# Optimization experiments

Hardware: AMD Instinct MI355X
Metric: run time of the kernel (lower is better)

## Reference

```python
import jax, jax.numpy as jnp
import numpy as np

N_NODES = 50000
N_EDGES = 800000
IN_DIM = 3
OUT_DIM = 50


def _glorot(key, shape):
    fan_in, fan_out = shape[0], shape[1]
    lim = np.sqrt(6.0 / (fan_in + fan_out))
    return jax.random.uniform(key, shape, jnp.float32, -lim, lim)


def setup_inputs() -> dict:
    key = jax.random.key(0)
    ks = jax.random.split(key, 16)
    x = jax.random.normal(ks[0], (N_NODES, IN_DIM), jnp.float32)
    edge_index = jax.random.randint(ks[1], (2, N_EDGES), 0, N_NODES, jnp.int64)
    return {
        "x": x,
        "edge_index": edge_index,
        # pointwise Conv1d (kernel_size=1) == per-node Linear; store as [in, out]
        "w1": _glorot(ks[2], (IN_DIM, 32)), "b1": jnp.zeros((32,), jnp.float32),
        "w2": _glorot(ks[3], (32, 64)),     "b2": jnp.zeros((64,), jnp.float32),
        "w3": _glorot(ks[4], (64, 128)),    "b3": jnp.zeros((128,), jnp.float32),
        # GCNConv weights [in, out] + bias
        "g1w": _glorot(ks[5], (128, 256)),  "g1b": jnp.zeros((256,), jnp.float32),
        "g2w": _glorot(ks[6], (256, 512)),  "g2b": jnp.zeros((512,), jnp.float32),
        "g3w": _glorot(ks[7], (512, OUT_DIM)), "g3b": jnp.zeros((OUT_DIM,), jnp.float32),
    }


def _gcn_conv(h, src, dst, dinv, W, b):
    """PyG GCNConv: add self-loops + symmetric norm. h: [N, Fin]."""
    n = h.shape[0]
    h = h @ W  # [N, Fout]
    norm = dinv[src] * dinv[dst]  # [E]
    msg = h[src] * norm[:, None]  # gather over edges [E, Fout]
    agg = jax.ops.segment_sum(msg, dst, num_segments=n)
    # self-loop contribution: norm = dinv[i]^2
    agg = agg + h * (dinv * dinv)[:, None]
    return agg + b


def reference(x, edge_index, w1, b1, w2, b2, w3, b3, g1w, g1b, g2w, g2b, g3w, g3b):
    src, dst = edge_index[0], edge_index[1]
    n = x.shape[0]
    # degree with self-loops (in-degree on targets), shared by all GCN layers
    deg = jnp.zeros((n,), x.dtype).at[dst].add(1.0) + 1.0
    dinv = jax.lax.rsqrt(deg)

    # pointwise conv stack (1x1 Conv1d == per-node dense layer)
    h = jax.nn.relu(x @ w1 + b1)
    h = jax.nn.relu(h @ w2 + b2)
    h = jax.nn.relu(h @ w3 + b3)

    h = jax.nn.relu(_gcn_conv(h, src, dst, dinv, g1w, g1b))
    h = jax.nn.relu(_gcn_conv(h, src, dst, dinv, g2w, g2b))
    h = _gcn_conv(h, src, dst, dinv, g3w, g3b)
    return jax.nn.softmax(h, axis=1)  # [N, OUT_DIM]
```

## Files before the change

### kernel.cpp

```cpp
#include <hip/hip_runtime.h>
#include <hip/hip_bf16.h>
#include <math.h>


typedef __attribute__((ext_vector_type(8))) short short8;
typedef __attribute__((ext_vector_type(8))) _Float16 half8;
typedef __attribute__((ext_vector_type(4))) float floatx4;

__device__ __forceinline__ unsigned short bf16h(float f) {
    unsigned int u = __float_as_uint(f);
    u += 0x7fff + ((u >> 16) & 1);
    return (unsigned short)(u >> 16);
}
__device__ __forceinline__ float bf16f(unsigned short h) {
    return __uint_as_float(((unsigned int)h) << 16);
}

__device__ __forceinline__ void gld_lds16(unsigned short* lds, const unsigned short* g) {
    __builtin_amdgcn_global_load_lds(
        (const __attribute__((address_space(1))) unsigned int*)g,
        (__attribute__((address_space(3))) unsigned int*)lds, 16, 0, 0);
}


__global__ void hist_kernel(const int* __restrict__ dst, int* __restrict__ counts, int e) {
    int g = blockIdx.x * blockDim.x + threadIdx.x;
    if (g < e) atomicAdd(&counts[dst[g]], 1);
}

__global__ void scan1_kernel(const int* __restrict__ counts, int* __restrict__ bsum, int n) {
    __shared__ int buf[256];
    int i = blockIdx.x * 256 + threadIdx.x;
    buf[threadIdx.x] = (i < n) ? counts[i] : 0;
    __syncthreads();
    for (int off = 128; off > 0; off >>= 1) {
        if (threadIdx.x < off) buf[threadIdx.x] += buf[threadIdx.x + off];
        __syncthreads();
    }
    if (threadIdx.x == 0) bsum[blockIdx.x] = buf[0];
}

__global__ void scan2_kernel(const int* __restrict__ bsum, int* __restrict__ bsumx,
                             int* __restrict__ offsets, int nb, int n) {
    __shared__ int buf[256];
    int tid = threadIdx.x;
    int v = (tid < nb) ? bsum[tid] : 0;
    buf[tid] = v;
    __syncthreads();
    for (int off = 1; off < 256; off <<= 1) {
        int t = (tid >= off) ? buf[tid - off] : 0;
        __syncthreads();
        buf[tid] += t;
        __syncthreads();
    }
    if (tid < nb) bsumx[tid] = buf[tid] - v;
    if (tid == 255) offsets[n] = buf[255];
}

__global__ void scan3_kernel(const int* __restrict__ counts, const int* __restrict__ bsumx,
                             int* __restrict__ offsets, int* __restrict__ cursor,
                             float* __restrict__ dinv, int n) {
    __shared__ int buf[256];
    int tid = threadIdx.x;
    int i = blockIdx.x * 256 + tid;
    int c = (i < n) ? counts[i] : 0;
    buf[tid] = c;
    __syncthreads();
    for (int off = 1; off < 256; off <<= 1) {
        int t = (tid >= off) ? buf[tid - off] : 0;
        __syncthreads();
        buf[tid] += t;
        __syncthreads();
    }
    if (i < n) {
        int excl = bsumx[blockIdx.x] + buf[tid] - c;
        offsets[i] = excl;
        cursor[i] = excl;
        dinv[i] = rsqrtf((float)c + 1.0f);
    }
}

__global__ void fill_kernel(const int* __restrict__ src, const int* __restrict__ dst,
                            const float* __restrict__ dinv, int* __restrict__ cursor,
                            int* __restrict__ ssrc, float* __restrict__ snorm, int e) {
    int g = blockIdx.x * blockDim.x + threadIdx.x;
    if (g >= e) return;
    int s = src[g], d = dst[g];
    int pos = atomicAdd(&cursor[d], 1);
    ssrc[pos]  = s;
    snorm[pos] = dinv[s] * dinv[d];
}


__global__ void prepw_kernel(const float* __restrict__ g1w, const float* __restrict__ g2w,
                             const float* __restrict__ g3w, const float* __restrict__ w3,
                             _Float16* __restrict__ Bt1f,
                             _Float16* __restrict__ Bt2f,
                             unsigned short* __restrict__ Bt3,
                             _Float16* __restrict__ Bt0f) {
    int gid = blockIdx.x * blockDim.x + threadIdx.x;
    if (gid < 32768) {
        int k = gid >> 8, n = gid & 255;
        Bt1f[(size_t)n * 128 + k] = (_Float16)g1w[gid];
    } else if (gid < 32768 + 131072) {
        int idx = gid - 32768;
        int k = idx >> 9, n = idx & 511;
        Bt2f[(size_t)n * 256 + k] = (_Float16)g2w[idx];
    } else if (gid < 32768 + 131072 + 32768) {
        int idx = gid - 32768 - 131072;
        int k = idx >> 6, c = idx & 63;
        float w = (c < 50) ? g3w[k * 50 + c] : 0.0f;
        unsigned short h = bf16h(w);
        unsigned short l = bf16h(w - bf16f(h));
        size_t base = (size_t)c * 1024;
        Bt3[base + k]       = h;
        Bt3[base + 512 + k] = l;
    } else if (gid < 32768 + 131072 + 32768 + 8192) {
        int idx = gid - 32768 - 131072 - 32768;
        int k = idx >> 7, n = idx & 127;
        Bt0f[(size_t)n * 64 + k] = (_Float16)w3[idx];
    }
}


__global__ __launch_bounds__(256) void mlp12_kernel(
        const float* __restrict__ x,
        const float* __restrict__ w1, const float* __restrict__ b1,
        const float* __restrict__ w2, const float* __restrict__ b2,
        _Float16* __restrict__ H2f, int n) {
    __shared__ float sw1[96], sb1[32], sw2[2048], sb2[64];
    int tid = threadIdx.x;
    if (tid < 96) sw1[tid] = w1[tid];
    if (tid < 32) sb1[tid] = b1[tid];
    if (tid < 64) sb2[tid] = b2[tid];
    for (int i = tid; i < 2048; i += 256) sw2[i] = w2[i];
    __syncthreads();

    int node = blockIdx.x * 256 + tid;
    if (node >= n) return;
    float x0 = x[node * 3 + 0], x1 = x[node * 3 + 1], x2 = x[node * 3 + 2];
    float h1[32];
#pragma unroll
    for (int j = 0; j < 32; j++)
        h1[j] = fmaxf(sb1[j] + x0 * sw1[j] + x1 * sw1[32 + j] + x2 * sw1[64 + j], 0.0f);

    float acc[64];
#pragma unroll
    for (int j = 0; j < 64; j++) acc[j] = sb2[j];
    for (int k = 0; k < 32; k++) {
        float hk = h1[k];
#pragma unroll
        for (int j4 = 0; j4 < 16; j4++) {
            float4 w = *(const float4*)&sw2[k * 64 + j4 * 4];
            acc[j4 * 4 + 0] = fmaf(hk, w.x, acc[j4 * 4 + 0]);
            acc[j4 * 4 + 1] = fmaf(hk, w.y, acc[j4 * 4 + 1]);
            acc[j4 * 4 + 2] = fmaf(hk, w.z, acc[j4 * 4 + 2]);
            acc[j4 * 4 + 3] = fmaf(hk, w.w, acc[j4 * 4 + 3]);
        }
    }
#pragma unroll
    for (int j8 = 0; j8 < 8; j8++) {
        half8 o;
#pragma unroll
        for (int t = 0; t < 8; t++)
            o[t] = (_Float16)fmaxf(acc[j8 * 8 + t], 0.0f);
        *reinterpret_cast<half8*>(&H2f[(size_t)node * 64 + j8 * 8]) = o;
    }
}


template<int BM, int BN, int WAVES, int WGR, int WGC, int WRF, int WCF, int SWIZCOLS>
__global__ __launch_bounds__(WAVES * 64) void gemm_f16_kernel(
        const _Float16* __restrict__ A, const _Float16* __restrict__ Btf,
        const float* __restrict__ bias, _Float16* __restrict__ C,
        int M, int K, int N) {
    static_assert(WGR * WRF * 16 == BM, "row cover");
    static_assert(WGC * WCF * 16 == BN, "col cover");
    static_assert(WGR * WGC == WAVES, "wave grid");
    constexpr int AUNITS = BM / 16, BUNITS = BN / 16;
    static_assert(AUNITS % WAVES == 0 && BUNITS % WAVES == 0, "staging split");
    __shared__ __align__(16) unsigned short Ash[BM * 32];
    __shared__ __align__(16) unsigned short Bsh[BN * 32];

    int bm, bn;
    if (SWIZCOLS > 0) {
        constexpr int CSH = (SWIZCOLS == 4) ? 2 : 1;
        int b = blockIdx.x;
        int col = (b >> 3) & (SWIZCOLS - 1);
        int row = ((b >> (3 + CSH)) << 3) | (b & 7);
        bm = row * BM;
        bn = col * BN;
        if (bm >= M) return;
    } else {
        bm = blockIdx.y * BM;
        bn = blockIdx.x * BN;
    }

    const int tid  = threadIdx.x;
    const int lane = tid & 63;
    const int wave = tid >> 6;
    const int wr0 = (wave / WGC) * (WRF * 16);
    const int wc0 = (wave % WGC) * (WCF * 16);
    const int lr   = lane & 15;
    const int quad = lane >> 4;
    const int arow = lane >> 2;
    const int acol = (lane & 3) * 8;

    floatx4 acc[WRF][WCF];
#pragma unroll
    for (int i = 0; i < WRF; i++)
#pragma unroll
        for (int j = 0; j < WCF; j++) acc[i][j] = floatx4{0.f, 0.f, 0.f, 0.f};

    for (int k0 = 0; k0 < K; k0 += 32) {
#pragma unroll
        for (int u = 0; u < AUNITS / WAVES; u++) {
            int grp = wave + u * WAVES;
            int gm = bm + grp * 16 + arow;
            if (gm >= M) gm = M - 1;
            gld_lds16(&Ash[grp * 512],
                      (const unsigned short*)(A + (size_t)gm * K + k0 + acol));
        }
#pragma unroll
        for (int u = 0; u < BUNITS / WAVES; u++) {
            int grp = wave + u * WAVES;
            int gr = bn + grp * 16 + arow;
            gld_lds16(&Bsh[grp * 512],
                      (const unsigned short*)(Btf + (size_t)gr * K + k0 + acol));
        }
        __syncthreads();

        half8 af[WRF], bf[WCF];
#pragma unroll
        for (int i = 0; i < WRF; i++)
            af[i] = *reinterpret_cast<const half8*>(
                &Ash[(wr0 + i * 16 + lr) * 32 + quad * 8]);
#pragma unroll
        for (int j = 0; j < WCF; j++)
            bf[j] = *reinterpret_cast<const half8*>(
                &Bsh[(wc0 + j * 16 + lr) * 32 + quad * 8]);
#pragma unroll
        for (int i = 0; i < WRF; i++)
#pragma unroll
            for (int j = 0; j < WCF; j++)
                acc[i][j] = __builtin_amdgcn_mfma_f32_16x16x32_f16(
                    af[i], bf[j], acc[i][j], 0, 0, 0);
        __syncthreads();
    }

#pragma unroll
    for (int i = 0; i < WRF; i++) {
#pragma unroll
        for (int j = 0; j < WCF; j++) {
            int gc = bn + wc0 + j * 16 + lr;
#pragma unroll
            for (int reg = 0; reg < 4; reg++) {
                int gr = bm + wr0 + i * 16 + quad * 4 + reg;
                if (gr >= M) continue;
                float v = fmaxf(acc[i][j][reg] + bias[gc], 0.0f);
                C[(size_t)gr * N + gc] = (_Float16)v;
            }
        }
    }
}


template<int BM, int BN, int WAVES, int WGR, int WGC, int WRF, int WCF>
__global__ __launch_bounds__(WAVES * 64) void gemm_emul_kernel(
        const _Float16* __restrict__ Af, const unsigned short* __restrict__ Bt,
        _Float16* __restrict__ C, int M, int K, int N) {
    static_assert(WGR * WRF * 16 == BM, "row cover");
    static_assert(WGC * WCF * 16 == BN, "col cover");
    static_assert(WGR * WGC == WAVES, "wave grid");
    constexpr int AUNITS = BM / 16, BUNITS = BN / 8;
    static_assert(AUNITS % WAVES == 0 && BUNITS % WAVES == 0, "staging split");
    __shared__ __align__(16) unsigned short Ash[BM * 32];
    __shared__ __align__(16) unsigned short Bsh[BN * 32];
    __shared__ __align__(16) unsigned short Bsl[BN * 32];

    const int bm = blockIdx.y * BM;
    const int bn = blockIdx.x * BN;
    const int tid  = threadIdx.x;
    const int lane = tid & 63;
    const int wave = tid >> 6;
    const int K2 = 2 * K;
    const int wr0 = (wave / WGC) * (WRF * 16);
    const int wc0 = (wave % WGC) * (WCF * 16);
    const int lr   = lane & 15;
    const int quad = lane >> 4;
    const int arow = lane >> 2;
    const int acol = (lane & 3) * 8;

    floatx4 acc[WRF][WCF];
#pragma unroll
    for (int i = 0; i < WRF; i++)
#pragma unroll
        for (int j = 0; j < WCF; j++) acc[i][j] = floatx4{0.f, 0.f, 0.f, 0.f};

    for (int k0 = 0; k0 < K; k0 += 32) {
#pragma unroll
        for (int u = 0; u < AUNITS / WAVES; u++) {
            int grp = wave + u * WAVES;
            int gm = bm + grp * 16 + arow;
            if (gm >= M) gm = M - 1;
            gld_lds16(&Ash[grp * 512],
                      (const unsigned short*)(Af + (size_t)gm * K + k0 + acol));
        }
#pragma unroll
        for (int u = 0; u < BUNITS / WAVES; u++) {
            int unit = wave + u * WAVES;
            int grp = unit >> 1, pl = unit & 1;
            int gr = bn + grp * 16 + arow;
            size_t go = (size_t)gr * K2 + k0 + acol + (pl ? K : 0);
            if (pl) gld_lds16(&Bsl[grp * 512], Bt + go);
            else    gld_lds16(&Bsh[grp * 512], Bt + go);
        }
        __syncthreads();

        short8 ahf[WRF], alf[WRF], bhf[WCF], blf[WCF];
#pragma unroll
        for (int i = 0; i < WRF; i++) {
            half8 av = *reinterpret_cast<const half8*>(
                &Ash[(wr0 + i * 16 + lr) * 32 + quad * 8]);
#pragma unroll
            for (int t = 0; t < 8; t++) {
                float f = (float)av[t];
                unsigned short h = bf16h(f);
                ahf[i][t] = (short)h;
                alf[i][t] = (short)bf16h(f - bf16f(h));
            }
        }
#pragma unroll
        for (int j = 0; j < WCF; j++) {
            int ro = (wc0 + j * 16 + lr) * 32 + quad * 8;
            bhf[j] = *reinterpret_cast<const short8*>(&Bsh[ro]);
            blf[j] = *reinterpret_cast<const short8*>(&Bsl[ro]);
        }
#pragma unroll
        for (int i = 0; i < WRF; i++)
#pragma unroll
            for (int j = 0; j < WCF; j++) {
                acc[i][j] = __builtin_amdgcn_mfma_f32_16x16x32_bf16(
                    ahf[i], bhf[j], acc[i][j], 0, 0, 0);
                acc[i][j] = __builtin_amdgcn_mfma_f32_16x16x32_bf16(
                    ahf[i], blf[j], acc[i][j], 0, 0, 0);
                acc[i][j] = __builtin_amdgcn_mfma_f32_16x16x32_bf16(
                    alf[i], bhf[j], acc[i][j], 0, 0, 0);
            }
        __syncthreads();
    }

#pragma unroll
    for (int i = 0; i < WRF; i++) {
#pragma unroll
        for (int j = 0; j < WCF; j++) {
            int gc = bn + wc0 + j * 16 + lr;
#pragma unroll
            for (int reg = 0; reg < 4; reg++) {
                int gr = bm + wr0 + i * 16 + quad * 4 + reg;
                if (gr >= M) continue;
                C[(size_t)gr * N + gc] = (_Float16)acc[i][j][reg];
            }
        }
    }
}


template<int F>
__global__ void agg_f16_kernel(const _Float16* __restrict__ table,
                               const int* __restrict__ offsets,
                               const int* __restrict__ ssrc,
                               const float* __restrict__ snorm,
                               const float* __restrict__ dinv,
                               _Float16* __restrict__ Aout, int n) {
    constexpr int F8 = F / 8;
    int gid = blockIdx.x * blockDim.x + threadIdx.x;
    if (gid >= n * F8) return;
    int node = gid / F8;
    int c8 = (gid - node * F8) * 8;

    float acc[8];
#pragma unroll
    for (int i = 0; i < 8; i++) acc[i] = 0.0f;

    int beg = offsets[node], end = offsets[node + 1];
    for (int e = beg; e < end; ++e) {
        int s = ssrc[e];
        float w = snorm[e];
        half8 r = *reinterpret_cast<const half8*>(table + (size_t)s * F + c8);
#pragma unroll
        for (int i = 0; i < 8; i++) acc[i] = fmaf((float)r[i], w, acc[i]);
    }
    float dv = dinv[node];
    float sw = dv * dv;
    half8 r = *reinterpret_cast<const half8*>(table + (size_t)node * F + c8);
#pragma unroll
    for (int i = 0; i < 8; i++) acc[i] = fmaf((float)r[i], sw, acc[i]);

    half8 o;
#pragma unroll
    for (int i = 0; i < 8; i++) o[i] = (_Float16)acc[i];
    *reinterpret_cast<half8*>(&Aout[(size_t)node * F + c8]) = o;
}


__global__ void agg50_softmax_kernel(const _Float16* __restrict__ z,
                                     const int* __restrict__ offsets,
                                     const int* __restrict__ ssrc,
                                     const float* __restrict__ snorm,
                                     const float* __restrict__ dinv,
                                     const float* __restrict__ bias,
                                     float* __restrict__ out, int n) {
    int node = blockIdx.x * 4 + (threadIdx.x >> 6);
    int lane = threadIdx.x & 63;
    if (node >= n) return;

    float a0 = 0.f, a1 = 0.f, a2 = 0.f, a3 = 0.f;
    int beg = offsets[node], end = offsets[node + 1];
    int e = beg;
    for (; e + 4 <= end; e += 4) {
        int s0 = ssrc[e + 0], s1 = ssrc[e + 1], s2 = ssrc[e + 2], s3 = ssrc[e + 3];
        float w0 = snorm[e + 0], w1 = snorm[e + 1];
        float w2 = snorm[e + 2], w3 = snorm[e + 3];
        float r0 = (float)z[(size_t)s0 * 64 + lane];
        float r1 = (float)z[(size_t)s1 * 64 + lane];
        float r2 = (float)z[(size_t)s2 * 64 + lane];
        float r3 = (float)z[(size_t)s3 * 64 + lane];
        a0 = fmaf(r0, w0, a0);
        a1 = fmaf(r1, w1, a1);
        a2 = fmaf(r2, w2, a2);
        a3 = fmaf(r3, w3, a3);
    }
    for (; e < end; ++e)
        a0 = fmaf((float)z[(size_t)ssrc[e] * 64 + lane], snorm[e], a0);

    float dv = dinv[node];
    float a = fmaf((float)z[(size_t)node * 64 + lane], dv * dv,
                   (a0 + a1) + (a2 + a3));

    float v = (lane < 50) ? a + bias[lane] : -INFINITY;
    float m = v;
#pragma unroll
    for (int off = 32; off > 0; off >>= 1) m = fmaxf(m, __shfl_xor(m, off));
    float ex = (lane < 50) ? expf(v - m) : 0.0f;
    float s = ex;
#pragma unroll
    for (int off = 32; off > 0; off >>= 1) s += __shfl_xor(s, off);
    if (lane < 50) out[(size_t)node * 50 + lane] = ex / s;
}


extern "C" void kernel_launch(void* const* d_in, const int* in_sizes, int n_in,
                              void* d_out, int out_size, void* d_ws, size_t ws_size,
                              hipStream_t stream) {
    const float* x    = (const float*)d_in[0];
    const int*   ei   = (const int*)  d_in[1];
    const float* w1   = (const float*)d_in[2];
    const float* b1   = (const float*)d_in[3];
    const float* w2   = (const float*)d_in[4];
    const float* b2   = (const float*)d_in[5];
    const float* w3   = (const float*)d_in[6];
    const float* b3   = (const float*)d_in[7];
    const float* g1w  = (const float*)d_in[8];
    const float* g1b  = (const float*)d_in[9];
    const float* g2w  = (const float*)d_in[10];
    const float* g2b  = (const float*)d_in[11];
    const float* g3w  = (const float*)d_in[12];
    const float* g3b  = (const float*)d_in[13];
    float* out = (float*)d_out;

    const int N = in_sizes[0] / 3;
    const int E = in_sizes[1] / 2;
    const int* src = ei;
    const int* dst = ei + E;
    const int NB = (N + 255) / 256;

    char* ws = (char*)d_ws;
    size_t off = 0;
    auto alloc = [&](size_t bytes) -> char* {
        char* p = ws + off;
        off = (off + bytes + 255) & ~(size_t)255;
        return p;
    };
    int*   counts  = (int*)  alloc((size_t)N * 4);
    int*   offsets = (int*)  alloc((size_t)(N + 1) * 4);
    int*   cursor  = (int*)  alloc((size_t)N * 4);
    float* dinv    = (float*)alloc((size_t)N * 4);
    int*   bsum    = (int*)  alloc((size_t)256 * 4);
    int*   bsumx   = (int*)  alloc((size_t)256 * 4);
    int*   ssrc    = (int*)  alloc((size_t)E * 4);
    float* snorm   = (float*)alloc((size_t)E * 4);
    _Float16* Bt1f = (_Float16*)alloc((size_t)256 * 128 * 2);
    _Float16* Bt2f = (_Float16*)alloc((size_t)512 * 256 * 2);
    unsigned short* Bt3 = (unsigned short*)alloc((size_t)64 * 1024 * 2);
    _Float16* Bt0f = (_Float16*)alloc((size_t)128 * 64 * 2);
    char* R1 = alloc((size_t)N * 256 * 4);
    char* R2 = alloc((size_t)N * 256 * 4);
    char* R3 = alloc((size_t)N * 512 * 2);
    (void)ws_size;

    _Float16*       S128f = (_Float16*)R1;
    _Float16*       A128f = (_Float16*)(R1 + (size_t)N * 128 * 2);
    _Float16*       A256f = (_Float16*)R1;
    _Float16*       H2f  = (_Float16*)R2;
    _Float16*       G1f  = (_Float16*)R2;
    _Float16*       zbuf = (_Float16*)R2;
    _Float16*       A512f = (_Float16*)R3;

    hipMemsetAsync(counts, 0, (size_t)N * 4, stream);
    hist_kernel<<<(E + 255) / 256, 256, 0, stream>>>(dst, counts, E);
    scan1_kernel<<<NB, 256, 0, stream>>>(counts, bsum, N);
    scan2_kernel<<<1, 256, 0, stream>>>(bsum, bsumx, offsets, NB, N);
    scan3_kernel<<<NB, 256, 0, stream>>>(counts, bsumx, offsets, cursor, dinv, N);
    fill_kernel<<<(E + 255) / 256, 256, 0, stream>>>(src, dst, dinv, cursor, ssrc, snorm, E);
    prepw_kernel<<<(204800 + 255) / 256, 256, 0, stream>>>(
        g1w, g2w, g3w, w3, Bt1f, Bt2f, Bt3, Bt0f);

    const int MB = (N + 127) / 128;
    const int MB8 = (MB + 7) & ~7;
    const int MB64 = (N + 63) / 64;

    mlp12_kernel<<<NB, 256, 0, stream>>>(x, w1, b1, w2, b2, H2f, N);
    {   dim3 grid(1, MB);
        gemm_f16_kernel<128, 128, 4, 2, 2, 4, 4, 0><<<grid, 256, 0, stream>>>(
            H2f, Bt0f, b3, S128f, N, 64, 128);
    }

    agg_f16_kernel<128><<<((size_t)N * 16 + 255) / 256, 256, 0, stream>>>(
        S128f, offsets, ssrc, snorm, dinv, A128f, N);
    gemm_f16_kernel<128, 128, 4, 2, 2, 4, 4, 2><<<2 * MB8, 256, 0, stream>>>(
        A128f, Bt1f, g1b, G1f, N, 128, 256);

    agg_f16_kernel<256><<<((size_t)N * 32 + 255) / 256, 256, 0, stream>>>(
        G1f, offsets, ssrc, snorm, dinv, A256f, N);
    gemm_f16_kernel<128, 128, 4, 2, 2, 4, 4, 4><<<4 * MB8, 256, 0, stream>>>(
        A256f, Bt2f, g2b, A512f, N, 256, 512);

    {   dim3 grid(1, MB64);
        gemm_emul_kernel<64, 64, 4, 4, 1, 1, 4><<<grid, 256, 0, stream>>>(
            A512f, Bt3, zbuf, N, 512, 64);
    }
    agg50_softmax_kernel<<<(N + 3) / 4, 256, 0, stream>>>(
        zbuf, offsets, ssrc, snorm, dinv, g3b, out, N);
}
```

Baseline: 453.9 us.

## Partition aggregation by feature slice per XCC with work-stealing queues and packed edges

After: 921.7 us. +103.1%, slower.

```diff
diff --git a/kernel.cpp b/kernel.cpp
--- a/kernel.cpp
+++ b/kernel.cpp
@@ -6,6 +6,8 @@
 typedef __attribute__((ext_vector_type(8))) short short8;
 typedef __attribute__((ext_vector_type(8))) _Float16 half8;
 typedef __attribute__((ext_vector_type(4))) float floatx4;
+
+#define XCC_ID_IMM 6164
 
 __device__ __forceinline__ unsigned short bf16h(float f) {
     unsigned int u = __float_as_uint(f);
@@ -82,13 +84,12 @@
 
 __global__ void fill_kernel(const int* __restrict__ src, const int* __restrict__ dst,
                             const float* __restrict__ dinv, int* __restrict__ cursor,
-                            int* __restrict__ ssrc, float* __restrict__ snorm, int e) {
+                            int2* __restrict__ edges, int e) {
     int g = blockIdx.x * blockDim.x + threadIdx.x;
     if (g >= e) return;
     int s = src[g], d = dst[g];
     int pos = atomicAdd(&cursor[d], 1);
-    ssrc[pos]  = s;
-    snorm[pos] = dinv[s] * dinv[d];
+    edges[pos] = make_int2(s, __float_as_int(dinv[s] * dinv[d]));
 }
 
 
@@ -367,47 +368,90 @@
 
 
 template<int F>
-__global__ void agg_f16_kernel(const _Float16* __restrict__ table,
-                               const int* __restrict__ offsets,
-                               const int* __restrict__ ssrc,
-                               const float* __restrict__ snorm,
-                               const float* __restrict__ dinv,
-                               _Float16* __restrict__ Aout, int n) {
-    constexpr int F8 = F / 8;
-    int gid = blockIdx.x * blockDim.x + threadIdx.x;
-    if (gid >= n * F8) return;
-    int node = gid / F8;
-    int c8 = (gid - node * F8) * 8;
-
-    float acc[8];
-#pragma unroll
-    for (int i = 0; i < 8; i++) acc[i] = 0.0f;
-
-    int beg = offsets[node], end = offsets[node + 1];
-    for (int e = beg; e < end; ++e) {
-        int s = ssrc[e];
-        float w = snorm[e];
-        half8 r = *reinterpret_cast<const half8*>(table + (size_t)s * F + c8);
-#pragma unroll
-        for (int i = 0; i < 8; i++) acc[i] = fmaf((float)r[i], w, acc[i]);
-    }
-    float dv = dinv[node];
-    float sw = dv * dv;
-    half8 r = *reinterpret_cast<const half8*>(table + (size_t)node * F + c8);
-#pragma unroll
-    for (int i = 0; i < 8; i++) acc[i] = fmaf((float)r[i], sw, acc[i]);
-
-    half8 o;
-#pragma unroll
-    for (int i = 0; i < 8; i++) o[i] = (_Float16)acc[i];
-    *reinterpret_cast<half8*>(&Aout[(size_t)node * F + c8]) = o;
+__global__ __launch_bounds__(256) void agg_slice_kernel(
+        const _Float16* __restrict__ table,
+        const int* __restrict__ offsets,
+        const int2* __restrict__ edges,
+        const float* __restrict__ dinv,
+        _Float16* __restrict__ Aout,
+        int* __restrict__ qheads, int n) {
+    constexpr int SF  = F / 8;
+    constexpr int LPN = SF / 8;
+    constexpr int NPB = 256 / LPN;
+    const int nslabs = (n + NPB - 1) / NPB;
+
+    __shared__ int sx, sslab;
+    const int tid = threadIdx.x;
+    if (tid == 0) sx = __builtin_amdgcn_s_getreg(XCC_ID_IMM) & 7;
+    __syncthreads();
+    const int myx = sx;
+    const int sub = tid & (LPN - 1);
+    const int nid = tid / LPN;
+
+    for (int t = 0; t < 8; t++) {
+        int q = (myx + t) & 7;
+        const int f0 = q * SF + sub * 8;
+        while (true) {
+            if (tid == 0) sslab = atomicAdd(&qheads[q], 1);
+            __syncthreads();
+            int slab = sslab;
+            __syncthreads();
+            if (slab >= nslabs) break;
+            int node = slab * NPB + nid;
+            if (node < n) {
+                float a0[8], a1[8];
+#pragma unroll
+                for (int i = 0; i < 8; i++) { a0[i] = 0.f; a1[i] = 0.f; }
+                int beg = offsets[node], end = offsets[node + 1];
+                int e = beg;
+                for (; e + 4 <= end; e += 4) {
+                    int2 E0 = edges[e + 0], E1 = edges[e + 1];
+                    int2 E2 = edges[e + 2], E3 = edges[e + 3];
+                    half8 r0 = *reinterpret_cast<const half8*>(
+                        table + (size_t)E0.x * F + f0);
+                    half8 r1 = *reinterpret_cast<const half8*>(
+                        table + (size_t)E1.x * F + f0);
+                    half8 r2 = *reinterpret_cast<const half8*>(
+                        table + (size_t)E2.x * F + f0);
+                    half8 r3 = *reinterpret_cast<const half8*>(
+                        table + (size_t)E3.x * F + f0);
+                    float w0 = __int_as_float(E0.y), w1 = __int_as_float(E1.y);
+                    float w2 = __int_as_float(E2.y), w3 = __int_as_float(E3.y);
+#pragma unroll
+                    for (int i = 0; i < 8; i++) {
+                        a0[i] = fmaf((float)r0[i], w0, a0[i]);
+                        a1[i] = fmaf((float)r1[i], w1, a1[i]);
+                        a0[i] = fmaf((float)r2[i], w2, a0[i]);
+                        a1[i] = fmaf((float)r3[i], w3, a1[i]);
+                    }
+                }
+                for (; e < end; ++e) {
+                    int2 E0 = edges[e];
+                    half8 r0 = *reinterpret_cast<const half8*>(
+                        table + (size_t)E0.x * F + f0);
+                    float w0 = __int_as_float(E0.y);
+#pragma unroll
+                    for (int i = 0; i < 8; i++)
+                        a0[i] = fmaf((float)r0[i], w0, a0[i]);
+                }
+                float dv = dinv[node];
+                float sw = dv * dv;
+                half8 rs = *reinterpret_cast<const half8*>(
+                    table + (size_t)node * F + f0);
+                half8 o;
+#pragma unroll
+                for (int i = 0; i < 8; i++)
+                    o[i] = (_Float16)fmaf((float)rs[i], sw, a0[i] + a1[i]);
+                *reinterpret_cast<half8*>(&Aout[(size_t)node * F + f0]) = o;
+            }
+        }
+    }
 }
 
 
 __global__ void agg50_softmax_kernel(const _Float16* __restrict__ z,
                                      const int* __restrict__ offsets,
-                                     const int* __restrict__ ssrc,
-                                     const float* __restrict__ snorm,
+                                     const int2* __restrict__ edges,
                                      const float* __restrict__ dinv,
                                      const float* __restrict__ bias,
                                      float* __restrict__ out, int n) {
@@ -419,20 +463,21 @@
     int beg = offsets[node], end = offsets[node + 1];
     int e = beg;
     for (; e + 4 <= end; e += 4) {
-        int s0 = ssrc[e + 0], s1 = ssrc[e + 1], s2 = ssrc[e + 2], s3 = ssrc[e + 3];
-        float w0 = snorm[e + 0], w1 = snorm[e + 1];
-        float w2 = snorm[e + 2], w3 = snorm[e + 3];
-        float r0 = (float)z[(size_t)s0 * 64 + lane];
-        float r1 = (float)z[(size_t)s1 * 64 + lane];
-        float r2 = (float)z[(size_t)s2 * 64 + lane];
-        float r3 = (float)z[(size_t)s3 * 64 + lane];
-        a0 = fmaf(r0, w0, a0);
-        a1 = fmaf(r1, w1, a1);
-        a2 = fmaf(r2, w2, a2);
-        a3 = fmaf(r3, w3, a3);
-    }
-    for (; e < end; ++e)
-        a0 = fmaf((float)z[(size_t)ssrc[e] * 64 + lane], snorm[e], a0);
+        int2 E0 = edges[e + 0], E1 = edges[e + 1];
+        int2 E2 = edges[e + 2], E3 = edges[e + 3];
+        float r0 = (float)z[(size_t)E0.x * 64 + lane];
+        float r1 = (float)z[(size_t)E1.x * 64 + lane];
+        float r2 = (float)z[(size_t)E2.x * 64 + lane];
+        float r3 = (float)z[(size_t)E3.x * 64 + lane];
+        a0 = fmaf(r0, __int_as_float(E0.y), a0);
+        a1 = fmaf(r1, __int_as_float(E1.y), a1);
+        a2 = fmaf(r2, __int_as_float(E2.y), a2);
+        a3 = fmaf(r3, __int_as_float(E3.y), a3);
+    }
+    for (; e < end; ++e) {
+        int2 E0 = edges[e];
+        a0 = fmaf((float)z[(size_t)E0.x * 64 + lane], __int_as_float(E0.y), a0);
+    }
 
     float dv = dinv[node];
     float a = fmaf((float)z[(size_t)node * 64 + lane], dv * dv,
@@ -483,13 +528,13 @@
         return p;
     };
     int*   counts  = (int*)  alloc((size_t)N * 4);
+    int*   qheads  = (int*)  alloc((size_t)16 * 4);
     int*   offsets = (int*)  alloc((size_t)(N + 1) * 4);
     int*   cursor  = (int*)  alloc((size_t)N * 4);
     float* dinv    = (float*)alloc((size_t)N * 4);
     int*   bsum    = (int*)  alloc((size_t)256 * 4);
     int*   bsumx   = (int*)  alloc((size_t)256 * 4);
-    int*   ssrc    = (int*)  alloc((size_t)E * 4);
-    float* snorm   = (float*)alloc((size_t)E * 4);
+    int2*  edges   = (int2*) alloc((size_t)E * 8);
     _Float16* Bt1f = (_Float16*)alloc((size_t)256 * 128 * 2);
     _Float16* Bt2f = (_Float16*)alloc((size_t)512 * 256 * 2);
     unsigned short* Bt3 = (unsigned short*)alloc((size_t)64 * 1024 * 2);
@@ -508,11 +553,12 @@
     _Float16*       A512f = (_Float16*)R3;
 
     hipMemsetAsync(counts, 0, (size_t)N * 4, stream);
+    hipMemsetAsync(qheads, 0, 64, stream);
     hist_kernel<<<(E + 255) / 256, 256, 0, stream>>>(dst, counts, E);
     scan1_kernel<<<NB, 256, 0, stream>>>(counts, bsum, N);
     scan2_kernel<<<1, 256, 0, stream>>>(bsum, bsumx, offsets, NB, N);
     scan3_kernel<<<NB, 256, 0, stream>>>(counts, bsumx, offsets, cursor, dinv, N);
-    fill_kernel<<<(E + 255) / 256, 256, 0, stream>>>(src, dst, dinv, cursor, ssrc, snorm, E);
+    fill_kernel<<<(E + 255) / 256, 256, 0, stream>>>(src, dst, dinv, cursor, edges, E);
     prepw_kernel<<<(204800 + 255) / 256, 256, 0, stream>>>(
         g1w, g2w, g3w, w3, Bt1f, Bt2f, Bt3, Bt0f);
 
@@ -526,13 +572,13 @@
             H2f, Bt0f, b3, S128f, N, 64, 128);
     }
 
-    agg_f16_kernel<128><<<((size_t)N * 16 + 255) / 256, 256, 0, stream>>>(
-        S128f, offsets, ssrc, snorm, dinv, A128f, N);
+    agg_slice_kernel<128><<<2048, 256, 0, stream>>>(
+        S128f, offsets, edges, dinv, A128f, qheads, N);
     gemm_f16_kernel<128, 128, 4, 2, 2, 4, 4, 2><<<2 * MB8, 256, 0, stream>>>(
         A128f, Bt1f, g1b, G1f, N, 128, 256);
 
-    agg_f16_kernel<256><<<((size_t)N * 32 + 255) / 256, 256, 0, stream>>>(
-        G1f, offsets, ssrc, snorm, dinv, A256f, N);
+    agg_slice_kernel<256><<<2048, 256, 0, stream>>>(
+        G1f, offsets, edges, dinv, A256f, qheads + 8, N);
     gemm_f16_kernel<128, 128, 4, 2, 2, 4, 4, 4><<<4 * MB8, 256, 0, stream>>>(
         A256f, Bt2f, g2b, A512f, N, 256, 512);
 
@@ -541,5 +587,5 @@
             A512f, Bt3, zbuf, N, 512, 64);
     }
     agg50_softmax_kernel<<<(N + 3) / 4, 256, 0, stream>>>(
-        zbuf, offsets, ssrc, snorm, dinv, g3b, out, N);
-}
+        zbuf, offsets, edges, dinv, g3b, out, N);
+}
```
